# Kernel tuning notes

Measured on AMD Instinct MI355X. Metric: run time of the kernel, lower is better.

The kernel has to match this reference:

```python
import jax, jax.numpy as jnp
import numpy as np

B, N, K, D, H, L = 2, 2048, 256, 768, 256, 64
REL_PROP = 3
NUM_BUCKETS = 64


def _pair_scores(u, dist_feat, left_w, left_b, right_w, right_b, out_w, out_b):
    # OptFFpairs-style pairwise scorer: left(u)_i + right(u)_j + dist_emb -> relu -> out
    left = jnp.einsum('bkd,hd->bkh', u, left_w) + left_b    # [B,K,H]
    right = jnp.einsum('bkd,hd->bkh', u, right_w) + right_b  # [B,K,H]
    h = jax.nn.relu(left[:, :, None, :] + right[:, None, :, :] + dist_feat)  # [B,K,K,H]
    return jnp.einsum('bijh,lh->bijl', h, out_w) + out_b     # [B,K,K,L]


def setup_inputs():
    key = jax.random.key(0)
    ks = jax.random.split(key, 12)
    s = 0.02
    all_span_vecs = jax.random.normal(ks[0], (B, N, D), dtype=jnp.float32)
    span_vecs = jax.random.normal(ks[1], (B, K, D), dtype=jnp.float32)
    span_begin = jnp.sort(jax.random.randint(ks[2], (B, K), 0, 1000), axis=-1).astype(jnp.int32)
    span_end = (span_begin + jax.random.randint(ks[3], (B, K), 1, 16)).astype(jnp.int32)
    square_mask = jnp.ones((B, K, K), dtype=jnp.float32)
    span_lengths = jnp.full((B,), float(K), dtype=jnp.float32)
    prune_indices = jnp.stack([
        jnp.sort(jax.random.choice(jax.random.fold_in(ks[4], b), N, (K,), replace=False))
        for b in range(B)
    ]).astype(jnp.int32)
    return {
        'all_span_vecs': all_span_vecs, 'span_vecs': span_vecs,
        'span_begin': span_begin, 'span_end': span_end,
        'square_mask': square_mask, 'span_lengths': span_lengths,
        'prune_indices': prune_indices,
        'left_w': jax.random.normal(ks[5], (H, D)) * s, 'left_b': jnp.zeros((H,), jnp.float32),
        'right_w': jax.random.normal(ks[6], (H, D)) * s, 'right_b': jnp.zeros((H,), jnp.float32),
        'dist_emb': jax.random.normal(ks[7], (NUM_BUCKETS, H)) * s,
        'out_w': jax.random.normal(ks[8], (L, H)) * s, 'out_b': jnp.zeros((L,), jnp.float32),
        'A_w': jax.random.normal(ks[9], (D, L)) * s,
        'B_w': jax.random.normal(ks[10], (D, L)) * s,
        'gate_w': jax.random.normal(ks[11], (D, 2 * D)) * s, 'gate_b': jnp.zeros((D,), jnp.float32),
    }


def reference(all_span_vecs, span_vecs, span_begin, span_end, square_mask, span_lengths,
              prune_indices, left_w, left_b, right_w, right_b, dist_emb, out_w, out_b,
              A_w, B_w, gate_w, gate_b):
    # distance-bucket embedding of the span pair (span_pair_generator)
    dist = span_begin[:, None, :] - span_end[:, :, None]                 # [B,K,K]
    buckets = jnp.clip(jnp.abs(dist), 0, NUM_BUCKETS - 1)
    dist_feat = dist_emb[buckets]                                        # [B,K,K,H]
    inv_len = 1.0 / span_lengths[:, None, None]                          # [B,1,1]

    update = span_vecs
    scores = _pair_scores(update, dist_feat, left_w, left_b, right_w, right_b, out_w, out_b)
    for _ in range(REL_PROP):
        probs = jax.nn.sigmoid(scores) * square_mask[..., None]          # [B,K,K,L]
        # torch: (A(probs) * update.unsqueeze(-2)).sum(-3) -> sum over i (rows)
        ctxt1 = jnp.einsum('bijl,dl,bid->bjd', probs, A_w, update) * inv_len
        # torch: (B(probs) * update.unsqueeze(-3)).sum(-2) -> sum over j (cols)
        ctxt2 = jnp.einsum('bijl,dl,bjd->bid', probs, B_w, update) * inv_len
        c = ctxt1 + ctxt2
        # MyGate: sigmoid-gated convex combination of old state and context
        g = jax.nn.sigmoid(jnp.concatenate([update, c], axis=-1) @ gate_w.T + gate_b)
        update = g * update + (1.0 - g) * c
        scores = _pair_scores(update, dist_feat, left_w, left_b, right_w, right_b, out_w, out_b)

    # overwrite_spans: scatter updated filtered spans back into the full span tensor
    valid = jnp.arange(K)[None, :] < span_lengths[:, None]               # [B,K]
    old = jnp.take_along_axis(all_span_vecs, prune_indices[..., None], axis=1)
    vals = jnp.where(valid[..., None], update, old)
    bidx = jnp.arange(B)[:, None]
    new_all = all_span_vecs.at[bidx, prune_indices].set(vals)
    return new_all, update, scores
```

## Files before the change

kernel.cpp:

```cpp
#include <hip/hip_runtime.h>

#define B_ 2
#define N_ 2048
#define K_ 256
#define D_ 768
#define H_ 256
#define L_ 64
#define BK_ (B_*K_)

typedef __attribute__((ext_vector_type(8))) __bf16 bf16x8;
typedef __attribute__((ext_vector_type(8))) unsigned short ushort8;
typedef __attribute__((ext_vector_type(4))) unsigned short ushort4v;
typedef __attribute__((ext_vector_type(4))) float f32x4;

__device__ __forceinline__ float sigm(float x) { return 1.0f / (1.0f + __expf(-x)); }

__device__ __forceinline__ unsigned short f2b(float f) {
    union { float f; unsigned int u; } v; v.f = f;
    unsigned int u = v.u;
    return (unsigned short)((u + 0x7FFFu + ((u >> 16) & 1u)) >> 16);
}
__device__ __forceinline__ unsigned short f2bc(float f) {
    __bf16 h = (__bf16)f;
    return __builtin_bit_cast(unsigned short, h);
}
__device__ __forceinline__ float b2f(unsigned short us) {
    union { unsigned int u; float f; } v; v.u = ((unsigned int)us) << 16;
    return v.f;
}
__device__ __forceinline__ bf16x8 ldb(const unsigned short* p) {
    ushort8 v = *(const ushort8*)p;
    return __builtin_bit_cast(bf16x8, v);
}
__device__ __forceinline__ bf16x8 cvt8(const float* p) {
    float4 v0 = *(const float4*)p;
    float4 v1 = *(const float4*)(p + 4);
    ushort8 u;
    u[0] = f2b(v0.x); u[1] = f2b(v0.y); u[2] = f2b(v0.z); u[3] = f2b(v0.w);
    u[4] = f2b(v1.x); u[5] = f2b(v1.y); u[6] = f2b(v1.z); u[7] = f2b(v1.w);
    return __builtin_bit_cast(bf16x8, u);
}

__global__ __launch_bounds__(256) void conv_all(
    const float* __restrict__ lw, const float* __restrict__ rw,
    const float* __restrict__ ow, const float* __restrict__ gw,
    const float* __restrict__ aw, const float* __restrict__ bw,
    const float* __restrict__ sv, const float* __restrict__ de,
    unsigned short* __restrict__ lwb, unsigned short* __restrict__ rwb,
    unsigned short* __restrict__ owb, unsigned short* __restrict__ gwb,
    unsigned short* __restrict__ wab, unsigned short* __restrict__ wbb,
    unsigned short* __restrict__ ub, unsigned short* __restrict__ deb)
{
    int i4 = (blockIdx.x * 256 + threadIdx.x) * 4;
    const float* src; unsigned short* dst; int off;
    if      (i4 <  196608) { src = lw; dst = lwb; off = 0; }
    else if (i4 <  393216) { src = rw; dst = rwb; off = 196608; }
    else if (i4 <  409600) { src = ow; dst = owb; off = 393216; }
    else if (i4 < 1589248) { src = gw; dst = gwb; off = 409600; }
    else if (i4 < 1638400) { src = aw; dst = wab; off = 1589248; }
    else if (i4 < 1687552) { src = bw; dst = wbb; off = 1638400; }
    else if (i4 < 2080768) { src = sv; dst = ub;  off = 1687552; }
    else if (i4 < 2097152) { src = de; dst = deb; off = 2080768; }
    else return;
    int j = i4 - off;
    float4 v = *(const float4*)&src[j];
    ushort4v p; p.x = f2b(v.x); p.y = f2b(v.y); p.z = f2b(v.z); p.w = f2b(v.w);
    *(ushort4v*)&dst[j] = p;
}

__global__ __launch_bounds__(64) void lr_mfma(
    const unsigned short* __restrict__ Ub,
    const unsigned short* __restrict__ lwb, const float* __restrict__ lb,
    const unsigned short* __restrict__ rwb, const float* __restrict__ rb,
    float* __restrict__ outL, float* __restrict__ outR)
{
    const int side = blockIdx.z;
    const unsigned short* __restrict__ W = side ? rwb : lwb;
    const float* __restrict__ bias = side ? rb : lb;
    float* __restrict__ outp = side ? outR : outL;
    const int r0 = blockIdx.x * 16, n0 = blockIdx.y * 64;
    const int lane = threadIdx.x;
    const int col = lane & 15, quad = lane >> 4;
    const unsigned short* arow = &Ub[(size_t)(r0 + col)*D_ + quad*8];
    f32x4 acc[4] = {};
    #pragma unroll 4
    for (int kc = 0; kc < D_; kc += 32) {
        bf16x8 a = ldb(arow + kc);
        #pragma unroll
        for (int nt = 0; nt < 4; ++nt) {
            bf16x8 bb = ldb(&W[(size_t)(n0 + nt*16 + col)*D_ + kc + quad*8]);
            acc[nt] = __builtin_amdgcn_mfma_f32_16x16x32_bf16(a, bb, acc[nt], 0, 0, 0);
        }
    }
    #pragma unroll
    for (int nt = 0; nt < 4; ++nt) {
        const int n = n0 + nt*16 + col;
        const float bv = bias[n];
        #pragma unroll
        for (int r = 0; r < 4; ++r) {
            const size_t idx = (size_t)(r0 + quad*4 + r)*H_ + n;
            outp[idx] = acc[nt][r] + bv;
        }
    }
}

__global__ __launch_bounds__(256, 2) void scores_v9(
    const float* __restrict__ leftb, const float* __restrict__ rightb,
    const int* __restrict__ span_begin, const int* __restrict__ span_end,
    const unsigned short* __restrict__ deb, const unsigned short* __restrict__ owb,
    const float* __restrict__ out_b, const float* __restrict__ mask,
    float* __restrict__ S, unsigned short* __restrict__ Pt, int writeP)
{
    const int j0 = blockIdx.x * 64;
    const int i0 = blockIdx.y * 8;
    const int b  = blockIdx.z;
    const int tid = threadIdx.x;
    const int w = tid >> 6, lane = tid & 63, col = lane & 15, quad = lane >> 4;
    const int jrow = w*16 + col;

    __shared__ unsigned short sDe[64][272];
    __shared__ float sL[8][256];
    __shared__ float sT[64][68];
    __shared__ float sMask[8][64];
    __shared__ int   sBkt[8][64];

    #pragma unroll
    for (int q = 0; q < 8; ++q) {
        int c = tid + q*256;
        int row = c >> 5, seg = (c & 31) * 8;
        *(ushort8*)&sDe[row][seg] = *(const ushort8*)&deb[row*H_ + seg];
    }
    #pragma unroll
    for (int q = 0; q < 2; ++q) {
        int p = tid + q*256;
        int ii = p >> 6, jj = p & 63;
        int d = span_begin[b*K_ + j0 + jj] - span_end[b*K_ + i0 + ii];
        if (d < 0) d = -d;
        sBkt[ii][jj] = d > 63 ? 63 : d;
        sMask[ii][jj] = mask[(size_t)(b*K_ + i0 + ii)*K_ + j0 + jj];
    }
    #pragma unroll
    for (int q = 0; q < 2; ++q) {
        int f = tid + q*256;
        int row = f >> 6, c4 = (f & 63) * 4;
        *(float4*)&sL[row][c4] = *(const float4*)&leftb[(size_t)(b*K_ + i0 + row)*H_ + c4];
    }
    __syncthreads();

    const unsigned short* sDeF = &sDe[0][0];
    int deoff[8];
    #pragma unroll
    for (int i = 0; i < 8; ++i) deoff[i] = sBkt[i][jrow] * 272;

    const float* rrow = &rightb[(size_t)(b*K_ + j0 + jrow)*H_ + quad*8];

    f32x4 acc[8][4] = {};
    #pragma unroll
    for (int k = 0; k < 8; ++k) {
        const float4 r0 = *(const float4*)&rrow[k*32];
        const float4 r1 = *(const float4*)&rrow[k*32 + 4];
        bf16x8 bbk[4];
        #pragma unroll
        for (int lt = 0; lt < 4; ++lt)
            bbk[lt] = ldb(&owb[(size_t)(lt*16 + col)*H_ + k*32 + quad*8]);
        #pragma unroll
        for (int i = 0; i < 8; ++i) {
            const ushort8 dv = *(const ushort8*)&sDeF[deoff[i] + k*32 + quad*8];
            const float* lr = &sL[i][k*32 + quad*8];
            const float4 l0 = *(const float4*)lr;
            const float4 l1 = *(const float4*)(lr + 4);
            bf16x8 a;
            a[0] = (__bf16)fmaxf(0.f, l0.x + r0.x + b2f(dv[0]));
            a[1] = (__bf16)fmaxf(0.f, l0.y + r0.y + b2f(dv[1]));
            a[2] = (__bf16)fmaxf(0.f, l0.z + r0.z + b2f(dv[2]));
            a[3] = (__bf16)fmaxf(0.f, l0.w + r0.w + b2f(dv[3]));
            a[4] = (__bf16)fmaxf(0.f, l1.x + r1.x + b2f(dv[4]));
            a[5] = (__bf16)fmaxf(0.f, l1.y + r1.y + b2f(dv[5]));
            a[6] = (__bf16)fmaxf(0.f, l1.z + r1.z + b2f(dv[6]));
            a[7] = (__bf16)fmaxf(0.f, l1.w + r1.w + b2f(dv[7]));
            #pragma unroll
            for (int lt = 0; lt < 4; ++lt)
                acc[i][lt] = __builtin_amdgcn_mfma_f32_16x16x32_bf16(a, bbk[lt], acc[i][lt], 0, 0, 0);
        }
    }

    float ob[4];
    #pragma unroll
    for (int lt = 0; lt < 4; ++lt) ob[lt] = out_b[lt*16 + col];

    #pragma unroll
    for (int i = 0; i < 8; ++i) {
        __syncthreads();
        #pragma unroll
        for (int lt = 0; lt < 4; ++lt)
            #pragma unroll
            for (int r = 0; r < 4; ++r)
                sT[w*16 + quad*4 + r][lt*16 + col] = acc[i][lt][r] + ob[lt];
        __syncthreads();
        const int jj = tid >> 2, seg = (tid & 3) * 16;
        const int j = j0 + jj, ii = i0 + i;
        if (writeP) {
            const float msk = sMask[i][jj];
            ushort8 o0, o1;
            #pragma unroll
            for (int e = 0; e < 8; ++e) {
                o0[e] = f2bc(sigm(sT[jj][seg + e]) * msk);
                o1[e] = f2bc(sigm(sT[jj][seg + 8 + e]) * msk);
            }
            unsigned short* dst = &Pt[(((size_t)b*K_ + j)*K_ + ii)*L_ + seg];
            *(ushort8*)&dst[0] = o0;
            *(ushort8*)&dst[8] = o1;
        } else {
            float* dst = &S[(((size_t)b*K_ + ii)*K_ + j)*L_ + seg];
            #pragma unroll
            for (int q2 = 0; q2 < 4; ++q2) {
                float4 v;
                v.x = sT[jj][seg + q2*4 + 0];
                v.y = sT[jj][seg + q2*4 + 1];
                v.z = sT[jj][seg + q2*4 + 2];
                v.w = sT[jj][seg + q2*4 + 3];
                *(float4*)&dst[q2*4] = v;
            }
        }
    }
}

__global__ __launch_bounds__(512, 4) void ctxt_v6(
    const unsigned short* __restrict__ Pt, const float* __restrict__ U,
    const unsigned short* __restrict__ WAb, const unsigned short* __restrict__ WBb,
    const float* __restrict__ lens, float* __restrict__ cacc)
{
    const int bid = blockIdx.x;
    const int m0 = (bid & 15) << 4;
    const int t0 = ((bid >> 4) & 7) << 5;
    const int mode = (bid >> 7) & 1;
    const int b = bid >> 8;
    const unsigned short* __restrict__ Wb = mode ? WBb : WAb;
    const int tid = threadIdx.x;
    const int w = tid >> 6, lane = tid & 63, col = lane & 15, quad = lane >> 4;
    const int dbase = w * 96;

    __shared__ unsigned short sP[2][16][72];
    __shared__ float sU[2][768];

    bf16x8 bw[6][2];
    #pragma unroll
    for (int dt = 0; dt < 6; ++dt)
        #pragma unroll
        for (int kc = 0; kc < 2; ++kc)
            bw[dt][kc] = ldb(&Wb[(size_t)(dbase + dt*16 + col)*L_ + kc*32 + quad*8]);

    const bool doP = tid < 128;
    const bool doU = (tid >= 128) && (tid < 320);
    const int prow = (tid & 127) >> 3, pseg = (tid & 7) * 8;
    const int ucol = (tid - 128) * 4;
    size_t pbase, tstep;
    if (mode) { pbase = (((size_t)b*K_ + t0)*K_ + m0 + prow)*L_ + pseg; tstep = (size_t)K_*L_; }
    else      { pbase = (((size_t)b*K_ + m0 + prow)*K_ + t0)*L_ + pseg; tstep = (size_t)L_; }

    ushort8 pv; float4 uv;
    if (doP) pv = *(const ushort8*)&Pt[pbase];
    if (doU) uv = *(const float4*)&U[((size_t)b*K_ + t0)*D_ + ucol];

    f32x4 acc[6] = {};
    for (int t = 0; t < 32; ++t) {
        unsigned short (*bp)[72] = sP[t & 1];
        float* bu = sU[t & 1];
        if (doP) *(ushort8*)&bp[prow][pseg] = pv;
        if (doU) *(float4*)&bu[ucol] = uv;
        __syncthreads();
        if (t < 31) {
            if (doP) pv = *(const ushort8*)&Pt[pbase + (size_t)(t + 1)*tstep];
            if (doU) uv = *(const float4*)&U[((size_t)b*K_ + t0 + t + 1)*D_ + ucol];
        }
        bf16x8 a0 = ldb(&bp[col][quad*8]);
        bf16x8 a1 = ldb(&bp[col][32 + quad*8]);
        #pragma unroll
        for (int dt = 0; dt < 6; ++dt) {
            f32x4 g = {0.f, 0.f, 0.f, 0.f};
            g = __builtin_amdgcn_mfma_f32_16x16x32_bf16(a0, bw[dt][0], g, 0, 0, 0);
            g = __builtin_amdgcn_mfma_f32_16x16x32_bf16(a1, bw[dt][1], g, 0, 0, 0);
            const float uu = bu[dbase + dt*16 + col];
            acc[dt] += g * uu;
        }
    }

    const float inv_len = 1.0f / lens[b];
    #pragma unroll
    for (int dt = 0; dt < 6; ++dt)
        #pragma unroll
        for (int r = 0; r < 4; ++r) {
            const int m = m0 + quad*4 + r;
            atomicAdd(&cacc[((size_t)(b*K_) + m)*D_ + dbase + dt*16 + col],
                      acc[dt][r] * inv_len);
        }
}

__global__ __launch_bounds__(64) void gate_mfma(
    const unsigned short* __restrict__ Ub, const unsigned short* __restrict__ gwb,
    const float* __restrict__ gb,
    const float* __restrict__ Ucur, const float* __restrict__ Cc,
    float* __restrict__ Unext, unsigned short* __restrict__ Ubnext)
{
    const int r0 = blockIdx.x * 16, n0 = blockIdx.y * 64;
    const int lane = threadIdx.x;
    const int col = lane & 15, quad = lane >> 4;
    const unsigned short* arow_u = &Ub[(size_t)(r0 + col)*D_ + quad*8];
    const float* arow_c = &Cc[(size_t)(r0 + col)*D_ + quad*8];
    f32x4 acc[4] = {};
    #pragma unroll 4
    for (int kc = 0; kc < D_; kc += 32) {
        bf16x8 a = ldb(arow_u + kc);
        #pragma unroll
        for (int nt = 0; nt < 4; ++nt) {
            bf16x8 bb = ldb(&gwb[(size_t)(n0 + nt*16 + col)*(2*D_) + kc + quad*8]);
            acc[nt] = __builtin_amdgcn_mfma_f32_16x16x32_bf16(a, bb, acc[nt], 0, 0, 0);
        }
    }
    #pragma unroll 4
    for (int kc = 0; kc < D_; kc += 32) {
        bf16x8 a = cvt8(arow_c + kc);
        #pragma unroll
        for (int nt = 0; nt < 4; ++nt) {
            bf16x8 bb = ldb(&gwb[(size_t)(n0 + nt*16 + col)*(2*D_) + D_ + kc + quad*8]);
            acc[nt] = __builtin_amdgcn_mfma_f32_16x16x32_bf16(a, bb, acc[nt], 0, 0, 0);
        }
    }
    #pragma unroll
    for (int nt = 0; nt < 4; ++nt) {
        const int n = n0 + nt*16 + col;
        const float gbv = gb[n];
        #pragma unroll
        for (int r = 0; r < 4; ++r) {
            const size_t idx = (size_t)(r0 + quad*4 + r)*D_ + n;
            const float gg = sigm(acc[nt][r] + gbv);
            const float o = gg * Ucur[idx] + (1.f - gg) * Cc[idx];
            Unext[idx] = o;
            Ubnext[idx] = f2b(o);
        }
    }
}

__global__ __launch_bounds__(256) void scatter_kernel(
    const float* __restrict__ upd, const int* __restrict__ prune,
    const float* __restrict__ lens, float* __restrict__ out_all)
{
    const int blk = blockIdx.x;
    const int b = blk / K_, k = blk % K_;
    if ((float)k < lens[b]) {
        const int pi = prune[b*K_ + k];
        const int tid = threadIdx.x;
        if (tid < D_/4) {
            float4 v = *(const float4*)&upd[((size_t)b*K_ + k)*D_ + tid*4];
            *(float4*)&out_all[((size_t)b*N_ + pi)*D_ + tid*4] = v;
        }
    }
}

extern "C" void kernel_launch(void* const* d_in, const int* in_sizes, int n_in,
                              void* d_out, int out_size, void* d_ws, size_t ws_size,
                              hipStream_t stream) {
    (void)in_sizes; (void)n_in; (void)out_size; (void)ws_size;
    const float* all_span_vecs = (const float*)d_in[0];
    const float* span_vecs     = (const float*)d_in[1];
    const int*   span_begin    = (const int*)d_in[2];
    const int*   span_end      = (const int*)d_in[3];
    const float* mask          = (const float*)d_in[4];
    const float* lens          = (const float*)d_in[5];
    const int*   prune         = (const int*)d_in[6];
    const float* lw  = (const float*)d_in[7];
    const float* lb  = (const float*)d_in[8];
    const float* rw  = (const float*)d_in[9];
    const float* rb  = (const float*)d_in[10];
    const float* dist_emb = (const float*)d_in[11];
    const float* out_w    = (const float*)d_in[12];
    const float* out_b    = (const float*)d_in[13];
    const float* A_w = (const float*)d_in[14];
    const float* B_w = (const float*)d_in[15];
    const float* gw  = (const float*)d_in[16];
    const float* gb  = (const float*)d_in[17];

    float* out_all = (float*)d_out;
    float* out_upd = out_all + (size_t)B_*N_*D_;
    float* out_sc  = out_upd + (size_t)BK_*D_;

    float* ws     = (float*)d_ws;
    float* leftb  = ws;
    float* rightf = leftb + (size_t)BK_*H_;
    float* U0     = rightf + (size_t)BK_*H_;
    float* U1     = U0 + (size_t)BK_*D_;
    float* cbuf   = U1 + (size_t)BK_*D_;
    unsigned short* WAb = (unsigned short*)(cbuf + (size_t)BK_*D_);
    unsigned short* WBb = WAb + (size_t)D_*L_;
    unsigned short* lwb = WBb + (size_t)D_*L_;
    unsigned short* rwb = lwb + (size_t)H_*D_;
    unsigned short* owb = rwb + (size_t)H_*D_;
    unsigned short* gwb = owb + (size_t)L_*H_;
    unsigned short* deb = gwb + (size_t)D_*2*D_;
    unsigned short* Ub0 = deb + (size_t)64*H_;
    unsigned short* Ub1 = Ub0 + (size_t)BK_*D_;
    unsigned short* Pt  = Ub1 + (size_t)BK_*D_;

    hipMemcpyAsync(out_all, all_span_vecs, sizeof(float)*(size_t)B_*N_*D_,
                   hipMemcpyDeviceToDevice, stream);

    dim3 blk256(256), blk64(64), blk512(512);
    conv_all<<<dim3(2048), blk256, 0, stream>>>(lw, rw, out_w, gw, A_w, B_w, span_vecs, dist_emb,
                                                lwb, rwb, owb, gwb, WAb, WBb, Ub0, deb);
    lr_mfma<<<dim3(BK_/16, H_/64, 2), blk64, 0, stream>>>(Ub0, lwb, lb, rwb, rb, leftb, rightf);
    scores_v9<<<dim3(K_/64, K_/8, B_), blk256, 0, stream>>>(leftb, rightf, span_begin, span_end,
                                                            deb, owb, out_b, mask,
                                                            out_sc, Pt, 1);
    const float* Ucur = span_vecs;
    const unsigned short* Ubcur = Ub0;
    float* nexts[3] = {U0, U1, out_upd};
    unsigned short* nextsUb[3] = {Ub1, Ub0, Ub1};
    for (int it = 0; it < 3; ++it) {
        hipMemsetAsync(cbuf, 0, sizeof(float)*(size_t)BK_*D_, stream);
        ctxt_v6<<<dim3(512), blk512, 0, stream>>>(Pt, Ucur, WAb, WBb, lens, cbuf);
        gate_mfma<<<dim3(BK_/16, D_/64), blk64, 0, stream>>>(Ubcur, gwb, gb,
                                                             Ucur, cbuf, nexts[it], nextsUb[it]);
        Ucur = nexts[it];
        Ubcur = nextsUb[it];
        lr_mfma<<<dim3(BK_/16, H_/64, 2), blk64, 0, stream>>>(Ubcur, lwb, lb, rwb, rb, leftb, rightf);
        scores_v9<<<dim3(K_/64, K_/8, B_), blk256, 0, stream>>>(leftb, rightf, span_begin, span_end,
                                                                deb, owb, out_b, mask,
                                                                out_sc, Pt, it == 2 ? 0 : 1);
    }
    scatter_kernel<<<dim3(BK_), blk256, 0, stream>>>(out_upd, prune, lens, out_all);
}
```

Measured before the change: 439.4 us.

## Shrink GEMM tiles for more blocks, pre-convert context to bf16, double-buffer ctxt loads

The lr and gate MFMA kernels now give each 64-thread block one 16x16 output tile instead of 16x64, which launches four times as many blocks so more of the GPU is busy on these small GEMMs. A new conv_c kernel converts the fp32 context buffer to bf16 once, so the gate kernel no longer converts it on the fly for every N tile. The ctxt kernel now keeps two prefetched P/U tiles in registers and alternates shared-memory buffers, putting more loads in flight. The costs are an extra kernel launch, an extra bf16 buffer, and A-row reloads repeated across four times as many blocks.

```diff
diff --git a/kernel.cpp b/kernel.cpp
--- a/kernel.cpp
+++ b/kernel.cpp
@@ -31,14 +31,6 @@
 __device__ __forceinline__ bf16x8 ldb(const unsigned short* p) {
     ushort8 v = *(const ushort8*)p;
     return __builtin_bit_cast(bf16x8, v);
-}
-__device__ __forceinline__ bf16x8 cvt8(const float* p) {
-    float4 v0 = *(const float4*)p;
-    float4 v1 = *(const float4*)(p + 4);
-    ushort8 u;
-    u[0] = f2b(v0.x); u[1] = f2b(v0.y); u[2] = f2b(v0.z); u[3] = f2b(v0.w);
-    u[4] = f2b(v1.x); u[5] = f2b(v1.y); u[6] = f2b(v1.z); u[7] = f2b(v1.w);
-    return __builtin_bit_cast(bf16x8, u);
 }
 
 __global__ __launch_bounds__(256) void conv_all(
@@ -68,7 +60,16 @@
     *(ushort4v*)&dst[j] = p;
 }
 
-__global__ __launch_bounds__(64) void lr_mfma(
+__global__ __launch_bounds__(256) void conv_c(
+    const float* __restrict__ c, unsigned short* __restrict__ cb)
+{
+    int i = (blockIdx.x * 256 + threadIdx.x) * 4;
+    float4 v = *(const float4*)&c[i];
+    ushort4v p; p.x = f2b(v.x); p.y = f2b(v.y); p.z = f2b(v.z); p.w = f2b(v.w);
+    *(ushort4v*)&cb[i] = p;
+}
+
+__global__ __launch_bounds__(64) void lr_mfma2(
     const unsigned short* __restrict__ Ub,
     const unsigned short* __restrict__ lwb, const float* __restrict__ lb,
     const unsigned short* __restrict__ rwb, const float* __restrict__ rb,
@@ -78,30 +79,23 @@
     const unsigned short* __restrict__ W = side ? rwb : lwb;
     const float* __restrict__ bias = side ? rb : lb;
     float* __restrict__ outp = side ? outR : outL;
-    const int r0 = blockIdx.x * 16, n0 = blockIdx.y * 64;
+    const int r0 = blockIdx.x * 16, n0 = blockIdx.y * 16;
     const int lane = threadIdx.x;
     const int col = lane & 15, quad = lane >> 4;
     const unsigned short* arow = &Ub[(size_t)(r0 + col)*D_ + quad*8];
-    f32x4 acc[4] = {};
-    #pragma unroll 4
+    const unsigned short* brow = &W[(size_t)(n0 + col)*D_ + quad*8];
+    f32x4 acc = {};
+    #pragma unroll
     for (int kc = 0; kc < D_; kc += 32) {
         bf16x8 a = ldb(arow + kc);
-        #pragma unroll
-        for (int nt = 0; nt < 4; ++nt) {
-            bf16x8 bb = ldb(&W[(size_t)(n0 + nt*16 + col)*D_ + kc + quad*8]);
-            acc[nt] = __builtin_amdgcn_mfma_f32_16x16x32_bf16(a, bb, acc[nt], 0, 0, 0);
-        }
-    }
-    #pragma unroll
-    for (int nt = 0; nt < 4; ++nt) {
-        const int n = n0 + nt*16 + col;
-        const float bv = bias[n];
-        #pragma unroll
-        for (int r = 0; r < 4; ++r) {
-            const size_t idx = (size_t)(r0 + quad*4 + r)*H_ + n;
-            outp[idx] = acc[nt][r] + bv;
-        }
-    }
+        bf16x8 bb = ldb(brow + kc);
+        acc = __builtin_amdgcn_mfma_f32_16x16x32_bf16(a, bb, acc, 0, 0, 0);
+    }
+    const int n = n0 + col;
+    const float bv = bias[n];
+    #pragma unroll
+    for (int r = 0; r < 4; ++r)
+        outp[(size_t)(r0 + quad*4 + r)*H_ + n] = acc[r] + bv;
 }
 
 __global__ __launch_bounds__(256, 2) void scores_v9(
@@ -225,7 +219,7 @@
     }
 }
 
-__global__ __launch_bounds__(512, 4) void ctxt_v6(
+__global__ __launch_bounds__(512, 4) void ctxt_v7(
     const unsigned short* __restrict__ Pt, const float* __restrict__ U,
     const unsigned short* __restrict__ WAb, const unsigned short* __restrict__ WBb,
     const float* __restrict__ lens, float* __restrict__ cacc)
@@ -258,32 +252,47 @@
     if (mode) { pbase = (((size_t)b*K_ + t0)*K_ + m0 + prow)*L_ + pseg; tstep = (size_t)K_*L_; }
     else      { pbase = (((size_t)b*K_ + m0 + prow)*K_ + t0)*L_ + pseg; tstep = (size_t)L_; }
 
-    ushort8 pv; float4 uv;
-    if (doP) pv = *(const ushort8*)&Pt[pbase];
-    if (doU) uv = *(const float4*)&U[((size_t)b*K_ + t0)*D_ + ucol];
+    ushort8 pvA, pvB; float4 uvA, uvB;
+    if (doP) { pvA = *(const ushort8*)&Pt[pbase];
+               pvB = *(const ushort8*)&Pt[pbase + tstep]; }
+    if (doU) { uvA = *(const float4*)&U[((size_t)b*K_ + t0)*D_ + ucol];
+               uvB = *(const float4*)&U[((size_t)b*K_ + t0 + 1)*D_ + ucol]; }
 
     f32x4 acc[6] = {};
-    for (int t = 0; t < 32; ++t) {
-        unsigned short (*bp)[72] = sP[t & 1];
-        float* bu = sU[t & 1];
-        if (doP) *(ushort8*)&bp[prow][pseg] = pv;
-        if (doU) *(float4*)&bu[ucol] = uv;
+
+    #define CTXT_COMPUTE(BUFI)                                                    \
+    {                                                                             \
+        bf16x8 a0 = ldb(&sP[BUFI][col][quad*8]);                                  \
+        bf16x8 a1 = ldb(&sP[BUFI][col][32 + quad*8]);                             \
+        _Pragma("unroll")                                                         \
+        for (int dt = 0; dt < 6; ++dt) {                                          \
+            f32x4 g = {0.f, 0.f, 0.f, 0.f};                                       \
+            g = __builtin_amdgcn_mfma_f32_16x16x32_bf16(a0, bw[dt][0], g, 0, 0, 0); \
+            g = __builtin_amdgcn_mfma_f32_16x16x32_bf16(a1, bw[dt][1], g, 0, 0, 0); \
+            const float uu = sU[BUFI][dbase + dt*16 + col];                       \
+            acc[dt] += g * uu;                                                    \
+        }                                                                         \
+    }
+
+    for (int t = 0; t < 32; t += 2) {
+        if (doP) *(ushort8*)&sP[0][prow][pseg] = pvA;
+        if (doU) *(float4*)&sU[0][ucol] = uvA;
         __syncthreads();
-        if (t < 31) {
-            if (doP) pv = *(const ushort8*)&Pt[pbase + (size_t)(t + 1)*tstep];
-            if (doU) uv = *(const float4*)&U[((size_t)b*K_ + t0 + t + 1)*D_ + ucol];
-        }
-        bf16x8 a0 = ldb(&bp[col][quad*8]);
-        bf16x8 a1 = ldb(&bp[col][32 + quad*8]);
-        #pragma unroll
-        for (int dt = 0; dt < 6; ++dt) {
-            f32x4 g = {0.f, 0.f, 0.f, 0.f};
-            g = __builtin_amdgcn_mfma_f32_16x16x32_bf16(a0, bw[dt][0], g, 0, 0, 0);
-            g = __builtin_amdgcn_mfma_f32_16x16x32_bf16(a1, bw[dt][1], g, 0, 0, 0);
-            const float uu = bu[dbase + dt*16 + col];
-            acc[dt] += g * uu;
-        }
-    }
+        if (t + 2 < 32) {
+            if (doP) pvA = *(const ushort8*)&Pt[pbase + (size_t)(t + 2)*tstep];
+            if (doU) uvA = *(const float4*)&U[((size_t)b*K_ + t0 + t + 2)*D_ + ucol];
+        }
+        CTXT_COMPUTE(0)
+        if (doP) *(ushort8*)&sP[1][prow][pseg] = pvB;
+        if (doU) *(float4*)&sU[1][ucol] = uvB;
+        __syncthreads();
+        if (t + 3 < 32) {
+            if (doP) pvB = *(const ushort8*)&Pt[pbase + (size_t)(t + 3)*tstep];
+            if (doU) uvB = *(const float4*)&U[((size_t)b*K_ + t0 + t + 3)*D_ + ucol];
+        }
+        CTXT_COMPUTE(1)
+    }
+    #undef CTXT_COMPUTE
 
     const float inv_len = 1.0f / lens[b];
     #pragma unroll
@@ -296,48 +305,40 @@
         }
 }
 
-__global__ __launch_bounds__(64) void gate_mfma(
-    const unsigned short* __restrict__ Ub, const unsigned short* __restrict__ gwb,
-    const float* __restrict__ gb,
+__global__ __launch_bounds__(64) void gate_mfma2(
+    const unsigned short* __restrict__ Ub, const unsigned short* __restrict__ cb,
+    const unsigned short* __restrict__ gwb, const float* __restrict__ gb,
     const float* __restrict__ Ucur, const float* __restrict__ Cc,
     float* __restrict__ Unext, unsigned short* __restrict__ Ubnext)
 {
-    const int r0 = blockIdx.x * 16, n0 = blockIdx.y * 64;
+    const int r0 = blockIdx.x * 16, n0 = blockIdx.y * 16;
     const int lane = threadIdx.x;
     const int col = lane & 15, quad = lane >> 4;
     const unsigned short* arow_u = &Ub[(size_t)(r0 + col)*D_ + quad*8];
-    const float* arow_c = &Cc[(size_t)(r0 + col)*D_ + quad*8];
-    f32x4 acc[4] = {};
-    #pragma unroll 4
+    const unsigned short* arow_c = &cb[(size_t)(r0 + col)*D_ + quad*8];
+    const unsigned short* brow   = &gwb[(size_t)(n0 + col)*(2*D_) + quad*8];
+    f32x4 acc = {};
+    #pragma unroll
     for (int kc = 0; kc < D_; kc += 32) {
         bf16x8 a = ldb(arow_u + kc);
-        #pragma unroll
-        for (int nt = 0; nt < 4; ++nt) {
-            bf16x8 bb = ldb(&gwb[(size_t)(n0 + nt*16 + col)*(2*D_) + kc + quad*8]);
-            acc[nt] = __builtin_amdgcn_mfma_f32_16x16x32_bf16(a, bb, acc[nt], 0, 0, 0);
-        }
-    }
-    #pragma unroll 4
+        bf16x8 bb = ldb(brow + kc);
+        acc = __builtin_amdgcn_mfma_f32_16x16x32_bf16(a, bb, acc, 0, 0, 0);
+    }
+    #pragma unroll
     for (int kc = 0; kc < D_; kc += 32) {
-        bf16x8 a = cvt8(arow_c + kc);
-        #pragma unroll
-        for (int nt = 0; nt < 4; ++nt) {
-            bf16x8 bb = ldb(&gwb[(size_t)(n0 + nt*16 + col)*(2*D_) + D_ + kc + quad*8]);
-            acc[nt] = __builtin_amdgcn_mfma_f32_16x16x32_bf16(a, bb, acc[nt], 0, 0, 0);
-        }
-    }
-    #pragma unroll
-    for (int nt = 0; nt < 4; ++nt) {
-        const int n = n0 + nt*16 + col;
-        const float gbv = gb[n];
-        #pragma unroll
-        for (int r = 0; r < 4; ++r) {
-            const size_t idx = (size_t)(r0 + quad*4 + r)*D_ + n;
-            const float gg = sigm(acc[nt][r] + gbv);
-            const float o = gg * Ucur[idx] + (1.f - gg) * Cc[idx];
-            Unext[idx] = o;
-            Ubnext[idx] = f2b(o);
-        }
+        bf16x8 a = ldb(arow_c + kc);
+        bf16x8 bb = ldb(brow + D_ + kc);
+        acc = __builtin_amdgcn_mfma_f32_16x16x32_bf16(a, bb, acc, 0, 0, 0);
+    }
+    const int n = n0 + col;
+    const float gbv = gb[n];
+    #pragma unroll
+    for (int r = 0; r < 4; ++r) {
+        const size_t idx = (size_t)(r0 + quad*4 + r)*D_ + n;
+        const float gg = sigm(acc[r] + gbv);
+        const float o = gg * Ucur[idx] + (1.f - gg) * Cc[idx];
+        Unext[idx] = o;
+        Ubnext[idx] = f2b(o);
     }
 }
 
@@ -399,7 +400,8 @@
     unsigned short* deb = gwb + (size_t)D_*2*D_;
     unsigned short* Ub0 = deb + (size_t)64*H_;
     unsigned short* Ub1 = Ub0 + (size_t)BK_*D_;
-    unsigned short* Pt  = Ub1 + (size_t)BK_*D_;
+    unsigned short* cb  = Ub1 + (size_t)BK_*D_;
+    unsigned short* Pt  = cb + (size_t)BK_*D_;
 
     hipMemcpyAsync(out_all, all_span_vecs, sizeof(float)*(size_t)B_*N_*D_,
                    hipMemcpyDeviceToDevice, stream);
@@ -407,7 +409,7 @@
     dim3 blk256(256), blk64(64), blk512(512);
     conv_all<<<dim3(2048), blk256, 0, stream>>>(lw, rw, out_w, gw, A_w, B_w, span_vecs, dist_emb,
                                                 lwb, rwb, owb, gwb, WAb, WBb, Ub0, deb);
-    lr_mfma<<<dim3(BK_/16, H_/64, 2), blk64, 0, stream>>>(Ub0, lwb, lb, rwb, rb, leftb, rightf);
+    lr_mfma2<<<dim3(BK_/16, H_/16, 2), blk64, 0, stream>>>(Ub0, lwb, lb, rwb, rb, leftb, rightf);
     scores_v9<<<dim3(K_/64, K_/8, B_), blk256, 0, stream>>>(leftb, rightf, span_begin, span_end,
                                                             deb, owb, out_b, mask,
                                                             out_sc, Pt, 1);
@@ -417,12 +419,13 @@
     unsigned short* nextsUb[3] = {Ub1, Ub0, Ub1};
     for (int it = 0; it < 3; ++it) {
         hipMemsetAsync(cbuf, 0, sizeof(float)*(size_t)BK_*D_, stream);
-        ctxt_v6<<<dim3(512), blk512, 0, stream>>>(Pt, Ucur, WAb, WBb, lens, cbuf);
-        gate_mfma<<<dim3(BK_/16, D_/64), blk64, 0, stream>>>(Ubcur, gwb, gb,
-                                                             Ucur, cbuf, nexts[it], nextsUb[it]);
+        ctxt_v7<<<dim3(512), blk512, 0, stream>>>(Pt, Ucur, WAb, WBb, lens, cbuf);
+        conv_c<<<dim3(BK_*D_/1024), blk256, 0, stream>>>(cbuf, cb);
+        gate_mfma2<<<dim3(BK_/16, D_/16), blk64, 0, stream>>>(Ubcur, cb, gwb, gb,
+                                                              Ucur, cbuf, nexts[it], nextsUb[it]);
         Ucur = nexts[it];
         Ubcur = nextsUb[it];
-        lr_mfma<<<dim3(BK_/16, H_/64, 2), blk64, 0, stream>>>(Ubcur, lwb, lb, rwb, rb, leftb, rightf);
+        lr_mfma2<<<dim3(BK_/16, H_/16, 2), blk64, 0, stream>>>(Ubcur, lwb, lb, rwb, rb, leftb, rightf);
         scores_v9<<<dim3(K_/64, K_/8, B_), blk256, 0, stream>>>(leftb, rightf, span_begin, span_end,
                                                                 deb, owb, out_b, mask,
                                                                 out_sc, Pt, it == 2 ? 0 : 1);
```

Result: faster. 428.8 us (-2.4%).
